# Kernel optimization log

Measured on AMD Instinct MI355X. Metric: run time of the kernel, lower is better.

The kernel has to match this reference:

```python
import jax, jax.numpy as jnp
import numpy as np

B, T, D, HD = 256, 256, 384, 64  # batch, seq_len, embedding_dim, head_dim


def setup_inputs() -> dict:
    key = jax.random.key(0)
    k1, k2, k3, k4 = jax.random.split(key, 4)
    x = jax.random.normal(k1, (B, T, D), dtype=jnp.float32)
    # nn.Linear(D, HD, bias=False) weight shape is [HD, D]; init scaled like kaiming-uniform magnitude
    Wq = jax.random.normal(k2, (HD, D), dtype=jnp.float32) * (1.0 / np.sqrt(D))
    Wk = jax.random.normal(k3, (HD, D), dtype=jnp.float32) * (1.0 / np.sqrt(D))
    Wv = jax.random.normal(k4, (HD, D), dtype=jnp.float32) * (1.0 / np.sqrt(D))
    return {"x": x, "Wq": Wq, "Wk": Wk, "Wv": Wv}


def reference(x, Wq, Wk, Wv):
    # Projections: x @ W^T  (Linear with bias=False)
    q = jnp.einsum('btd,hd->bth', x, Wq)  # [B,T,HD]
    k = jnp.einsum('btd,hd->bth', x, Wk)
    v = jnp.einsum('btd,hd->bth', x, Wv)
    scale = 1.0 / np.sqrt(HD).astype(np.float32)
    scores = jnp.einsum('bqh,bkh->bqk', q, k) * scale  # [B,T,T]
    T_ = x.shape[1]
    causal = jnp.tril(jnp.ones((T_, T_), dtype=bool))
    scores = jnp.where(causal, scores, jnp.float32(-jnp.inf))
    attn = jax.nn.softmax(scores, axis=-1)
    # dropout disabled (eval mode) for deterministic reference
    return jnp.einsum('bqk,bkh->bqh', attn, v)
```

## Files before the change

### kernel.cpp

```cpp
#include <hip/hip_runtime.h>

typedef __attribute__((ext_vector_type(8))) short bf16x8;
typedef __attribute__((ext_vector_type(4))) float f32x4;

__device__ inline unsigned short f2bf(float f) {
    unsigned u = __float_as_uint(f);
    return (unsigned short)((u + 0x7fffu + ((u >> 16) & 1u)) >> 16);
}

__device__ inline void gload16(const void* g, void* l) {
    __builtin_amdgcn_global_load_lds(
        (const __attribute__((address_space(1))) unsigned*)g,
        (__attribute__((address_space(3))) unsigned*)l, 16, 0, 0);
}

__global__ void wconv(const float* __restrict__ Wq, const float* __restrict__ Wk,
                      const float* __restrict__ Wv, short* __restrict__ Wp) {
    int i = blockIdx.x * 256 + threadIdx.x;
    if (i >= 192 * 384) return;
    int col = i / 384;
    int k   = i - col * 384;
    const float* src = col < 64 ? (Wq + col * 384)
                     : col < 128 ? (Wk + (col - 64) * 384)
                                 : (Wv + (col - 128) * 384);
    int kc = k >> 5, g = (k >> 3) & 3, kl = k & 7;
    Wp[kc * 6144 + (((g * 192 + col) ^ g) << 3) + kl] = (short)f2bf(src[k]);
}

__global__ __launch_bounds__(1024) void fused_attn(
    const float* __restrict__ x, const short* __restrict__ Wp,
    float* __restrict__ out) {
    __shared__ short LDSH[45568];
    short* const Ksh = LDSH;
    short* const Vt  = LDSH + 18432;
    short* const Pb  = LDSH + 35328;
    short* const wst = LDSH;
    short* const xst = LDSH + 18432;

    const int tid = threadIdx.x;
    const int wv = tid >> 6, lane = tid & 63;
    const int g = lane >> 4, c = lane & 15;
    const int b = blockIdx.x;
    const int q0 = wv * 16;

    const int xr0 = tid >> 3;
    const int xc4 = tid & 7;
    const float* gx0 = x + ((size_t)b * 256 + xr0) * 384 + xc4 * 4;
    const float* gx1 = gx0 + (size_t)128 * 384;

    f32x4 acc[12];
#pragma unroll
    for (int j = 0; j < 12; ++j) acc[j] = (f32x4){0.f, 0.f, 0.f, 0.f};

#define STAGE_W(S, BUF)                                                       \
    if (wv < 12) gload16(Wp + (S) * 6144 + wv * 512 + lane * 8,               \
                         wst + (BUF) * 6144 + wv * 512);
#define XWRITE(BUF, A, Bv)                                                    \
    {                                                                         \
        uint2 p0_, p1_;                                                       \
        p0_.x = (unsigned)f2bf((A).x) | ((unsigned)f2bf((A).y) << 16);        \
        p0_.y = (unsigned)f2bf((A).z) | ((unsigned)f2bf((A).w) << 16);        \
        p1_.x = (unsigned)f2bf((Bv).x) | ((unsigned)f2bf((Bv).y) << 16);      \
        p1_.y = (unsigned)f2bf((Bv).z) | ((unsigned)f2bf((Bv).w) << 16);      \
        *(uint2*)&xst[(BUF) * 10240 + xr0 * 40 + xc4 * 4] = p0_;              \
        *(uint2*)&xst[(BUF) * 10240 + (xr0 + 128) * 40 + xc4 * 4] = p1_;      \
    }

    STAGE_W(0, 0)
    {
        float4 a0 = *(const float4*)(gx0);
        float4 a1 = *(const float4*)(gx1);
        XWRITE(0, a0, a1)
    }
    asm volatile("s_waitcnt vmcnt(0)" ::: "memory");
    __syncthreads();

    for (int s = 0; s < 12; ++s) {
        float4 na0, na1;
        if (s < 11) {
            na0 = *(const float4*)(gx0 + (s + 1) * 32);
            na1 = *(const float4*)(gx1 + (s + 1) * 32);
            STAGE_W(s + 1, (s + 1) & 1)
        }
        const short* xb = xst + (s & 1) * 10240;
        const short* wb = wst + (s & 1) * 6144;
        bf16x8 af = *(const bf16x8*)&xb[(q0 + c) * 40 + g * 8];
#pragma unroll
        for (int h_ = 0; h_ < 2; ++h_) {
            bf16x8 bfr[6];
#pragma unroll
            for (int j6 = 0; j6 < 6; ++j6) {
                int col = (h_ * 6 + j6) * 16 + c;
                bfr[j6] = *(const bf16x8*)&wb[((g * 192 + col) ^ g) << 3];
            }
#pragma unroll
            for (int j6 = 0; j6 < 6; ++j6)
                acc[h_ * 6 + j6] = __builtin_amdgcn_mfma_f32_16x16x32_bf16(
                    af, bfr[j6], acc[h_ * 6 + j6], 0, 0, 0);
        }
        if (s < 11) XWRITE((s + 1) & 1, na0, na1)
        asm volatile("s_waitcnt vmcnt(0)" ::: "memory");
        __syncthreads();
    }

    short* const pbw = Pb + wv * 640;
    bf16x8 qf0, qf1;
    {
#pragma unroll
        for (int r = 0; r < 4; ++r) {
            pbw[(4 * g + r) * 40 + c]      = (short)f2bf(acc[0][r]);
            pbw[(4 * g + r) * 40 + 16 + c] = (short)f2bf(acc[1][r]);
        }
        qf0 = *(const bf16x8*)&pbw[c * 40 + g * 8];
#pragma unroll
        for (int r = 0; r < 4; ++r) {
            pbw[(4 * g + r) * 40 + c]      = (short)f2bf(acc[2][r]);
            pbw[(4 * g + r) * 40 + 16 + c] = (short)f2bf(acc[3][r]);
        }
        qf1 = *(const bf16x8*)&pbw[c * 40 + g * 8];
    }
#pragma unroll
    for (int nj = 4; nj < 8; ++nj) {
        const int row = q0 + 4 * g;
#pragma unroll
        for (int r = 0; r < 4; ++r)
            Ksh[(row + r) * 72 + (nj - 4) * 16 + c] = (short)f2bf(acc[nj][r]);
    }
#pragma unroll
    for (int nj = 8; nj < 12; ++nj) {
        const int h = (nj - 8) * 16 + c;
        const int swz = ((h >> 3) & 7) << 3;
        const int row = q0 + 4 * g;
#pragma unroll
        for (int r = 0; r < 4; ++r)
            Vt[(h * 264 + row + r) ^ swz] = (short)f2bf(acc[nj][r]);
    }
    __syncthreads();

    {
        f32x4 o[4];
#pragma unroll
        for (int nj = 0; nj < 4; ++nj) o[nj] = (f32x4){0.f, 0.f, 0.f, 0.f};
        float m[4] = {-INFINITY, -INFINITY, -INFINITY, -INFINITY};
        float ls[4] = {0.f, 0.f, 0.f, 0.f};
        const int jmax = (q0 + 15) >> 5;

        for (int j = 0; j <= jmax; ++j) {
            f32x4 s0 = {0.f, 0.f, 0.f, 0.f}, s1 = {0.f, 0.f, 0.f, 0.f};
            {
                bf16x8 kf;
                kf = *(const bf16x8*)&Ksh[(32 * j + c) * 72 + g * 8];
                s0 = __builtin_amdgcn_mfma_f32_16x16x32_bf16(qf0, kf, s0, 0, 0, 0);
                kf = *(const bf16x8*)&Ksh[(32 * j + c) * 72 + 32 + g * 8];
                s0 = __builtin_amdgcn_mfma_f32_16x16x32_bf16(qf1, kf, s0, 0, 0, 0);
                kf = *(const bf16x8*)&Ksh[(32 * j + 16 + c) * 72 + g * 8];
                s1 = __builtin_amdgcn_mfma_f32_16x16x32_bf16(qf0, kf, s1, 0, 0, 0);
                kf = *(const bf16x8*)&Ksh[(32 * j + 16 + c) * 72 + 32 + g * 8];
                s1 = __builtin_amdgcn_mfma_f32_16x16x32_bf16(qf1, kf, s1, 0, 0, 0);
            }
            float t0[4], t1[4];
#pragma unroll
            for (int r = 0; r < 4; ++r) {
                t0[r] = s0[r] * 0.125f;
                t1[r] = s1[r] * 0.125f;
            }
            if (j == jmax) {
                int q = q0 + 4 * g;
#pragma unroll
                for (int r = 0; r < 4; ++r) {
                    if (32 * j + c > q + r) t0[r] = -INFINITY;
                    if (32 * j + 16 + c > q + r) t1[r] = -INFINITY;
                }
            }
            float corr[4], p0[4], p1[4];
#pragma unroll
            for (int r = 0; r < 4; ++r) {
                float v = fmaxf(t0[r], t1[r]);
#pragma unroll
                for (int off = 1; off < 16; off <<= 1) v = fmaxf(v, __shfl_xor(v, off, 16));
                float mn = fmaxf(m[r], v);
                corr[r] = __expf(m[r] - mn);
                m[r] = mn;
                p0[r] = __expf(t0[r] - mn);
                p1[r] = __expf(t1[r] - mn);
                float rs = p0[r] + p1[r];
#pragma unroll
                for (int off = 1; off < 16; off <<= 1) rs += __shfl_xor(rs, off, 16);
                ls[r] = ls[r] * corr[r] + rs;
            }
#pragma unroll
            for (int nj = 0; nj < 4; ++nj) {
                f32x4 t = o[nj];
                t[0] *= corr[0]; t[1] *= corr[1]; t[2] *= corr[2]; t[3] *= corr[3];
                o[nj] = t;
            }
#pragma unroll
            for (int r = 0; r < 4; ++r) {
                pbw[(4 * g + r) * 40 + c]      = (short)f2bf(p0[r]);
                pbw[(4 * g + r) * 40 + 16 + c] = (short)f2bf(p1[r]);
            }
            bf16x8 pfa = *(const bf16x8*)&pbw[c * 40 + g * 8];
#pragma unroll
            for (int nj = 0; nj < 4; ++nj) {
                int h = 16 * nj + c;
                int swz = ((2 * nj + (c >> 3)) & 7) << 3;
                bf16x8 vf = *(const bf16x8*)&Vt[(h * 264 + 32 * j + g * 8) ^ swz];
                o[nj] = __builtin_amdgcn_mfma_f32_16x16x32_bf16(pfa, vf, o[nj], 0, 0, 0);
            }
        }
        float inv[4];
#pragma unroll
        for (int r = 0; r < 4; ++r) inv[r] = 1.f / ls[r];
        float* ob = out + ((size_t)b * 256 + q0) * 64;
#pragma unroll
        for (int nj = 0; nj < 4; ++nj)
#pragma unroll
            for (int r = 0; r < 4; ++r)
                ob[(4 * g + r) * 64 + 16 * nj + c] = o[nj][r] * inv[r];
    }
#undef STAGE_W
#undef XWRITE
}

extern "C" void kernel_launch(void* const* d_in, const int* in_sizes, int n_in,
                              void* d_out, int out_size, void* d_ws, size_t ws_size,
                              hipStream_t stream) {
    const float* x  = (const float*)d_in[0];
    const float* Wq = (const float*)d_in[1];
    const float* Wk = (const float*)d_in[2];
    const float* Wv = (const float*)d_in[3];
    float* out = (float*)d_out;

    short* Wp = (short*)d_ws;

    wconv<<<dim3(288), dim3(256), 0, stream>>>(Wq, Wk, Wv, Wp);
    fused_attn<<<dim3(256), dim3(1024), 0, stream>>>(x, Wp, out);
}
```

Before: 42.75 us.

## Deepen x prefetch to two stages with rotating registers and partial vmcnt waits

The projection K-loop is fully unrolled with three rotating register sets for x, so global loads of x are issued two stages ahead rather than one. The full vmcnt(0) drain at each step becomes vmcnt(2), which lets the next x loads stay in flight across the barrier. Sched barriers pin the order of issue. This is meant to hide global latency for x in the projection phase, at the cost of more registers and larger code.

```diff
diff --git a/kernel.cpp b/kernel.cpp
--- a/kernel.cpp
+++ b/kernel.cpp
@@ -7,7 +7,6 @@
     unsigned u = __float_as_uint(f);
     return (unsigned short)((u + 0x7fffu + ((u >> 16) & 1u)) >> 16);
 }
-
 __device__ inline void gload16(const void* g, void* l) {
     __builtin_amdgcn_global_load_lds(
         (const __attribute__((address_space(1))) unsigned*)g,
@@ -65,43 +64,74 @@
         *(uint2*)&xst[(BUF) * 10240 + xr0 * 40 + xc4 * 4] = p0_;              \
         *(uint2*)&xst[(BUF) * 10240 + (xr0 + 128) * 40 + xc4 * 4] = p1_;      \
     }
-
+#define COMPUTE(S)                                                            \
+    {                                                                         \
+        const short* xb = xst + ((S) & 1) * 10240;                            \
+        const short* wb = wst + ((S) & 1) * 6144;                             \
+        bf16x8 af = *(const bf16x8*)&xb[(q0 + c) * 40 + g * 8];               \
+        _Pragma("unroll")                                                     \
+        for (int h_ = 0; h_ < 2; ++h_) {                                      \
+            bf16x8 bfr[6];                                                    \
+            _Pragma("unroll")                                                 \
+            for (int j6 = 0; j6 < 6; ++j6) {                                  \
+                int col = (h_ * 6 + j6) * 16 + c;                             \
+                bfr[j6] = *(const bf16x8*)&wb[((g * 192 + col) ^ g) << 3];    \
+            }                                                                 \
+            _Pragma("unroll")                                                 \
+            for (int j6 = 0; j6 < 6; ++j6)                                    \
+                acc[h_ * 6 + j6] = __builtin_amdgcn_mfma_f32_16x16x32_bf16(   \
+                    af, bfr[j6], acc[h_ * 6 + j6], 0, 0, 0);                  \
+    }                                                                         \
+    }
+#define STEP(S, LX0, LX1, WX0, WX1)                                          \
+    {                                                                        \
+        STAGE_W((S) + 1, ((S) + 1) & 1)                                      \
+        __builtin_amdgcn_sched_barrier(0);                                   \
+        if ((S) <= 9) {                                                      \
+            LX0 = *(const float4*)(gx0 + ((S) + 2) * 32);                    \
+            LX1 = *(const float4*)(gx1 + ((S) + 2) * 32);                    \
+        }                                                                    \
+        __builtin_amdgcn_sched_barrier(0);                                   \
+        COMPUTE(S)                                                           \
+        XWRITE(((S) + 1) & 1, WX0, WX1)                                      \
+        if (wv < 12) {                                                       \
+            if ((S) <= 9) asm volatile("s_waitcnt vmcnt(2)" ::: "memory");   \
+            else          asm volatile("s_waitcnt vmcnt(0)" ::: "memory");   \
+        }                                                                    \
+        asm volatile("s_waitcnt lgkmcnt(0)" ::: "memory");                   \
+        __builtin_amdgcn_s_barrier();                                        \
+        __builtin_amdgcn_sched_barrier(0);                                   \
+    }
+
+    float4 xA0, xA1, xB0, xB1, xC0, xC1;
+
+    xA0 = *(const float4*)(gx0);
+    xA1 = *(const float4*)(gx1);
+    __builtin_amdgcn_sched_barrier(0);
     STAGE_W(0, 0)
-    {
-        float4 a0 = *(const float4*)(gx0);
-        float4 a1 = *(const float4*)(gx1);
-        XWRITE(0, a0, a1)
-    }
-    asm volatile("s_waitcnt vmcnt(0)" ::: "memory");
+    __builtin_amdgcn_sched_barrier(0);
+    xB0 = *(const float4*)(gx0 + 32);
+    xB1 = *(const float4*)(gx1 + 32);
+    __builtin_amdgcn_sched_barrier(0);
+    XWRITE(0, xA0, xA1)
+    if (wv < 12) asm volatile("s_waitcnt vmcnt(2)" ::: "memory");
+    asm volatile("s_waitcnt lgkmcnt(0)" ::: "memory");
+    __builtin_amdgcn_s_barrier();
+    __builtin_amdgcn_sched_barrier(0);
+
+    STEP(0, xC0, xC1, xB0, xB1)
+    STEP(1, xA0, xA1, xC0, xC1)
+    STEP(2, xB0, xB1, xA0, xA1)
+    STEP(3, xC0, xC1, xB0, xB1)
+    STEP(4, xA0, xA1, xC0, xC1)
+    STEP(5, xB0, xB1, xA0, xA1)
+    STEP(6, xC0, xC1, xB0, xB1)
+    STEP(7, xA0, xA1, xC0, xC1)
+    STEP(8, xB0, xB1, xA0, xA1)
+    STEP(9, xC0, xC1, xB0, xB1)
+    STEP(10, xA0, xA1, xC0, xC1)
+    COMPUTE(11)
     __syncthreads();
-
-    for (int s = 0; s < 12; ++s) {
-        float4 na0, na1;
-        if (s < 11) {
-            na0 = *(const float4*)(gx0 + (s + 1) * 32);
-            na1 = *(const float4*)(gx1 + (s + 1) * 32);
-            STAGE_W(s + 1, (s + 1) & 1)
-        }
-        const short* xb = xst + (s & 1) * 10240;
-        const short* wb = wst + (s & 1) * 6144;
-        bf16x8 af = *(const bf16x8*)&xb[(q0 + c) * 40 + g * 8];
-#pragma unroll
-        for (int h_ = 0; h_ < 2; ++h_) {
-            bf16x8 bfr[6];
-#pragma unroll
-            for (int j6 = 0; j6 < 6; ++j6) {
-                int col = (h_ * 6 + j6) * 16 + c;
-                bfr[j6] = *(const bf16x8*)&wb[((g * 192 + col) ^ g) << 3];
-            }
-#pragma unroll
-            for (int j6 = 0; j6 < 6; ++j6)
-                acc[h_ * 6 + j6] = __builtin_amdgcn_mfma_f32_16x16x32_bf16(
-                    af, bfr[j6], acc[h_ * 6 + j6], 0, 0, 0);
-        }
-        if (s < 11) XWRITE((s + 1) & 1, na0, na1)
-        asm volatile("s_waitcnt vmcnt(0)" ::: "memory");
-        __syncthreads();
-    }
 
     short* const pbw = Pb + wv * 640;
     bf16x8 qf0, qf1;
@@ -220,6 +250,8 @@
     }
 #undef STAGE_W
 #undef XWRITE
+#undef COMPUTE
+#undef STEP
 }
 
 extern "C" void kernel_launch(void* const* d_in, const int* in_sizes, int n_in,
```

New measurement: 41.10 us. 3.9% less time.
